# Kernel optimization log

Measured on AMD Instinct MI355X. Metric: run time of the kernel, lower is better.

## Reference

```python
import jax, jax.numpy as jnp
import numpy as np

B = 131072       # batch of sentences
L = 64           # padded paragraph length
N_TOPICS = 81    # topics 0..80 (range(81) in the original)


def setup_inputs() -> dict:
    key = jax.random.key(0)
    k1, k2, k3 = jax.random.split(key, 3)
    P = jax.random.uniform(k1, (B, N_TOPICS), dtype=jnp.float32)
    # -1 is the padding value; valid topic ids are in [0, 81)
    hard_label = jax.random.randint(k2, (B, L), -1, N_TOPICS, dtype=jnp.int64)
    sent_idx = jax.random.randint(k3, (B,), 0, 32, dtype=jnp.int64)
    return {"P": P, "hard_label": hard_label, "sent_idx": sent_idx}


def reference(P, hard_label, sent_idx):
    # mask1 = hard_label >= 0; mask1[0:sent_idx] = False
    pos = jnp.arange(L)
    mask = (hard_label >= 0) & (pos[None, :] >= sent_idx[:, None])  # [B, L]
    # set membership over topics 0..80: scatter masked labels into slot 81 (dump)
    valid = jnp.where(mask, hard_label, N_TOPICS)  # [B, L], invalid -> 81
    member = jnp.zeros((B, N_TOPICS + 1), dtype=bool)
    member = member.at[jnp.arange(B)[:, None], valid].set(True)[:, :N_TOPICS]  # [B, 81]
    # max_prob starts at 0 and only updated when P[i] > max_prob -> max(0, masked max)
    max_prob = jnp.max(jnp.where(member, P, 0.0), axis=1, initial=0.0)  # [B]
    return -max_prob
```

## Files before the change

kernel.cpp:

```cpp
#include <hip/hip_runtime.h>
#include <hip/hip_bf16.h>

#define L_LEN 64
#define N_TOPICS 81
#define ROW_STRIDE 84
#define ROWS_PER_WAVE 8
#define WAVES_PER_BLOCK 4
#define ROWS_PER_BLOCK 32

__global__ __launch_bounds__(256) void rangeshrink_max_kernel(
    const float* __restrict__ P,
    const int* __restrict__ hard_label,
    const int* __restrict__ sent_idx,
    float* __restrict__ out,
    int nrows)
{
    __shared__ float member[ROWS_PER_BLOCK * ROW_STRIDE];

    const int wave = threadIdx.x >> 6;
    const int lane = threadIdx.x & 63;
    const int g    = lane >> 3;
    const int lig  = lane & 7;

    const int localRow = wave * ROWS_PER_WAVE + g;
    const int row = blockIdx.x * ROWS_PER_BLOCK + localRow;
    if (row >= nrows) return;

    const float* __restrict__ Prow = P + (size_t)row * N_TOPICS;
    float pv[11];
    #pragma unroll
    for (int t = 0; t < 11; ++t) {
        const int idx = lig + 8 * t;
        pv[t] = (idx <= 80) ? Prow[idx] : 0.0f;
    }

    const int4* __restrict__ hl4 = (const int4*)hard_label;
    const int4 la = hl4[(size_t)row * 16 + lig * 2];
    const int4 lb = hl4[(size_t)row * 16 + lig * 2 + 1];
    const int si = sent_idx[row];

    float* const mwave = member + (wave * ROWS_PER_WAVE) * ROW_STRIDE;
    #pragma unroll
    for (int t = 0; t < 11; ++t) {
        const int d = lane + 64 * t;
        if (d < ROWS_PER_WAVE * ROW_STRIDE) mwave[d] = 0.0f;
    }
    __builtin_amdgcn_wave_barrier();

    float* const srow = member + localRow * ROW_STRIDE;
    const int labs[8] = { la.x, la.y, la.z, la.w, lb.x, lb.y, lb.z, lb.w };
    #pragma unroll
    for (int k = 0; k < 8; ++k) {
        const int j = lig * 8 + k;
        if (j >= si && labs[k] >= 0) srow[labs[k]] = 1.0f;
    }
    __builtin_amdgcn_wave_barrier();

    const float* const mrow = member + localRow * ROW_STRIDE;
    float v = 0.0f;
    #pragma unroll
    for (int t = 0; t < 11; ++t) {
        const int idx = lig + 8 * t;
        if (idx <= 80) v = fmaxf(v, mrow[idx] * pv[t]);
    }

    #pragma unroll
    for (int off = 1; off < 8; off <<= 1) {
        v = fmaxf(v, __shfl_xor(v, off, 64));
    }

    if (lig == 0) out[row] = -v;
}

extern "C" void kernel_launch(void* const* d_in, const int* in_sizes, int n_in,
                              void* d_out, int out_size, void* d_ws, size_t ws_size,
                              hipStream_t stream) {
    const float* P          = (const float*)d_in[0];
    const int*   hard_label = (const int*)d_in[1];
    const int*   sent_idx   = (const int*)d_in[2];
    float*       out        = (float*)d_out;

    const int nrows = out_size;
    const int grid = (nrows + ROWS_PER_BLOCK - 1) / ROWS_PER_BLOCK;

    rangeshrink_max_kernel<<<grid, 256, 0, stream>>>(P, hard_label, sent_idx, out, nrows);
}
```

Baseline: 17.13 us.

## Replace shared-memory membership table with register bitmasks and float4 P loads

Builds the topic membership set as three 32-bit register bitmasks, OR-reduced across the 8 lanes of each row with shuffles, which removes the shared-memory zeroing, scatter and readback. P rows are now read as aligned float4 vectors from a 16-byte-aligned base, and the mask is shifted by the row's misalignment so each lane can pick its 4-bit nibble per vector. This cuts LDS traffic and the number of load instructions, but adds shift and bit arithmetic plus extra shuffles, and relies on careful bounds logic for the final row.

```diff
diff --git a/kernel.cpp b/kernel.cpp
--- a/kernel.cpp
+++ b/kernel.cpp
@@ -3,9 +3,7 @@
 
 #define L_LEN 64
 #define N_TOPICS 81
-#define ROW_STRIDE 84
 #define ROWS_PER_WAVE 8
-#define WAVES_PER_BLOCK 4
 #define ROWS_PER_BLOCK 32
 
 __global__ __launch_bounds__(256) void rangeshrink_max_kernel(
@@ -15,58 +13,77 @@
     float* __restrict__ out,
     int nrows)
 {
-    __shared__ float member[ROWS_PER_BLOCK * ROW_STRIDE];
-
     const int wave = threadIdx.x >> 6;
     const int lane = threadIdx.x & 63;
     const int g    = lane >> 3;
     const int lig  = lane & 7;
 
-    const int localRow = wave * ROWS_PER_WAVE + g;
-    const int row = blockIdx.x * ROWS_PER_BLOCK + localRow;
+    const int row = blockIdx.x * ROWS_PER_BLOCK + wave * ROWS_PER_WAVE + g;
     if (row >= nrows) return;
 
-    const float* __restrict__ Prow = P + (size_t)row * N_TOPICS;
-    float pv[11];
-    #pragma unroll
-    for (int t = 0; t < 11; ++t) {
-        const int idx = lig + 8 * t;
-        pv[t] = (idx <= 80) ? Prow[idx] : 0.0f;
-    }
+    const size_t base_dw = (size_t)row * N_TOPICS;
+    const int    off     = row & 3;
+    const size_t a0      = base_dw - off;
+    const float4* __restrict__ W4 = (const float4*)(P + a0);
+
+    const int f2 = lig + 16;
+    const bool ok2 = (f2 <= 20) && ((row < nrows - 1) || (4 * f2 + 3 <= 80 + off));
+
+    float4 p0 = W4[lig];
+    float4 p1 = W4[lig + 8];
+    float4 p2 = ok2 ? W4[f2] : make_float4(0.f, 0.f, 0.f, 0.f);
 
     const int4* __restrict__ hl4 = (const int4*)hard_label;
     const int4 la = hl4[(size_t)row * 16 + lig * 2];
     const int4 lb = hl4[(size_t)row * 16 + lig * 2 + 1];
-    const int si = sent_idx[row];
+    const int  si = sent_idx[row];
 
-    float* const mwave = member + (wave * ROWS_PER_WAVE) * ROW_STRIDE;
-    #pragma unroll
-    for (int t = 0; t < 11; ++t) {
-        const int d = lane + 64 * t;
-        if (d < ROWS_PER_WAVE * ROW_STRIDE) mwave[d] = 0.0f;
-    }
-    __builtin_amdgcn_wave_barrier();
-
-    float* const srow = member + localRow * ROW_STRIDE;
+    unsigned m0 = 0u, m1 = 0u, m2 = 0u;
     const int labs[8] = { la.x, la.y, la.z, la.w, lb.x, lb.y, lb.z, lb.w };
     #pragma unroll
     for (int k = 0; k < 8; ++k) {
-        const int j = lig * 8 + k;
-        if (j >= si && labs[k] >= 0) srow[labs[k]] = 1.0f;
-    }
-    __builtin_amdgcn_wave_barrier();
-
-    const float* const mrow = member + localRow * ROW_STRIDE;
-    float v = 0.0f;
-    #pragma unroll
-    for (int t = 0; t < 11; ++t) {
-        const int idx = lig + 8 * t;
-        if (idx <= 80) v = fmaxf(v, mrow[idx] * pv[t]);
+        const int j   = lig * 8 + k;
+        const int lab = labs[k];
+        const bool valid = (j >= si) && (lab >= 0);
+        const unsigned b = 1u << (lab & 31);
+        const int w = lab >> 5;
+        m0 |= (valid && w == 0) ? b : 0u;
+        m1 |= (valid && w == 1) ? b : 0u;
+        m2 |= (valid && w == 2) ? b : 0u;
     }
 
     #pragma unroll
-    for (int off = 1; off < 8; off <<= 1) {
-        v = fmaxf(v, __shfl_xor(v, off, 64));
+    for (int o = 1; o < 8; o <<= 1) {
+        m0 |= __shfl_xor(m0, o, 64);
+        m1 |= __shfl_xor(m1, o, 64);
+        m2 |= __shfl_xor(m2, o, 64);
+    }
+
+    const unsigned long long lo = (unsigned long long)m0 | ((unsigned long long)m1 << 32);
+    const unsigned long long hi = (unsigned long long)m1 | ((unsigned long long)m2 << 32);
+    const unsigned long long slo = lo << off;
+    const unsigned s0 = (unsigned)slo;
+    const unsigned s1 = (unsigned)(slo >> 32);
+    const unsigned s2 = (unsigned)((hi << off) >> 32);
+
+    const unsigned n0 = (s0 >> (4 * lig)) & 0xFu;
+    const unsigned n1 = (s1 >> (4 * lig)) & 0xFu;
+    const unsigned n2 = (s2 >> (4 * lig)) & 0xFu;
+
+    float v = 0.0f;
+    const float e0[4] = { p0.x, p0.y, p0.z, p0.w };
+    const float e1[4] = { p1.x, p1.y, p1.z, p1.w };
+    const float e2[4] = { p2.x, p2.y, p2.z, p2.w };
+    #pragma unroll
+    for (int e = 0; e < 4; ++e) {
+        v = fmaxf(v, ((n0 >> e) & 1u) ? e0[e] : 0.0f);
+        v = fmaxf(v, ((n1 >> e) & 1u) ? e1[e] : 0.0f);
+        v = fmaxf(v, ((n2 >> e) & 1u) ? e2[e] : 0.0f);
+    }
+
+    #pragma unroll
+    for (int o = 1; o < 8; o <<= 1) {
+        v = fmaxf(v, __shfl_xor(v, o, 64));
     }
 
     if (lig == 0) out[row] = -v;
```

After: 18.01 us. +5.1%, slower.

## Stage P rows in LDS and gather by label instead of building membership mask

Applied to the files above, without the earlier changes.

Each row's P values are now loaded with aligned float4 reads and written into LDS, and each lane gathers P at its masked labels directly, taking the max. This removes the membership-mask zeroing pass, the scattered flag writes and one wave barrier, and replaces scalar P loads with vector loads. In exchange it adds boundary logic for unaligned row starts, including an over-read guard on the last row, and a trash slot that absorbs out-of-range stores.

```diff
diff --git a/kernel.cpp b/kernel.cpp
--- a/kernel.cpp
+++ b/kernel.cpp
@@ -1,12 +1,12 @@
 #include <hip/hip_runtime.h>
 #include <hip/hip_bf16.h>
 
-#define L_LEN 64
 #define N_TOPICS 81
-#define ROW_STRIDE 84
 #define ROWS_PER_WAVE 8
-#define WAVES_PER_BLOCK 4
 #define ROWS_PER_BLOCK 32
+#define ROW_STRIDE 88
+#define ZERO_SLOT 84
+#define TRASH_SLOT 86
 
 __global__ __launch_bounds__(256) void rangeshrink_max_kernel(
     const float* __restrict__ P,
@@ -15,7 +15,7 @@
     float* __restrict__ out,
     int nrows)
 {
-    __shared__ float member[ROWS_PER_BLOCK * ROW_STRIDE];
+    __shared__ float lds[ROWS_PER_BLOCK * ROW_STRIDE];
 
     const int wave = threadIdx.x >> 6;
     const int lane = threadIdx.x & 63;
@@ -26,47 +26,52 @@
     const int row = blockIdx.x * ROWS_PER_BLOCK + localRow;
     if (row >= nrows) return;
 
-    const float* __restrict__ Prow = P + (size_t)row * N_TOPICS;
-    float pv[11];
-    #pragma unroll
-    for (int t = 0; t < 11; ++t) {
-        const int idx = lig + 8 * t;
-        pv[t] = (idx <= 80) ? Prow[idx] : 0.0f;
-    }
+    const size_t base_dw = (size_t)row * N_TOPICS;
+    const int    off     = (int)(base_dw & 3);
+    const float4* __restrict__ W4 = (const float4*)(P + (base_dw - off));
+
+    float4 p0 = W4[lig];
+    float4 p1 = W4[lig + 8];
+    float4 p2 = make_float4(0.f, 0.f, 0.f, 0.f);
+    const bool ok2 = (lig <= 4) && ((row < nrows - 1) || (off == 3));
+    if (ok2) p2 = W4[lig + 16];
 
     const int4* __restrict__ hl4 = (const int4*)hard_label;
     const int4 la = hl4[(size_t)row * 16 + lig * 2];
     const int4 lb = hl4[(size_t)row * 16 + lig * 2 + 1];
-    const int si = sent_idx[row];
+    const int  si = sent_idx[row];
 
-    float* const mwave = member + (wave * ROWS_PER_WAVE) * ROW_STRIDE;
+    float* const srow = lds + localRow * ROW_STRIDE;
+    if (lig == 0) srow[ZERO_SLOT] = 0.0f;
+
+    const int d0 = lig * 4 - off;
+    const float pe0[4] = { p0.x, p0.y, p0.z, p0.w };
+    const float pe1[4] = { p1.x, p1.y, p1.z, p1.w };
+    const float pe2[4] = { p2.x, p2.y, p2.z, p2.w };
     #pragma unroll
-    for (int t = 0; t < 11; ++t) {
-        const int d = lane + 64 * t;
-        if (d < ROWS_PER_WAVE * ROW_STRIDE) mwave[d] = 0.0f;
+    for (int e = 0; e < 4; ++e) {
+        const int t0 = d0 + e;
+        srow[((unsigned)t0 <= 80u) ? t0 : TRASH_SLOT] = pe0[e];
+        const int t1 = d0 + 32 + e;
+        srow[t1] = pe1[e];
+        const int t2 = d0 + 64 + e;
+        srow[((unsigned)t2 <= 80u) ? t2 : TRASH_SLOT] = pe2[e];
     }
     __builtin_amdgcn_wave_barrier();
 
-    float* const srow = member + localRow * ROW_STRIDE;
+    const int base = lig * 8 - si;
     const int labs[8] = { la.x, la.y, la.z, la.w, lb.x, lb.y, lb.z, lb.w };
+    float v = 0.0f;
     #pragma unroll
     for (int k = 0; k < 8; ++k) {
-        const int j = lig * 8 + k;
-        if (j >= si && labs[k] >= 0) srow[labs[k]] = 1.0f;
-    }
-    __builtin_amdgcn_wave_barrier();
-
-    const float* const mrow = member + localRow * ROW_STRIDE;
-    float v = 0.0f;
-    #pragma unroll
-    for (int t = 0; t < 11; ++t) {
-        const int idx = lig + 8 * t;
-        if (idx <= 80) v = fmaxf(v, mrow[idx] * pv[t]);
+        const int m   = (base + k) | labs[k];
+        const int idx = (m < 0) ? ZERO_SLOT : labs[k];
+        v = fmaxf(v, srow[idx]);
     }
 
     #pragma unroll
-    for (int off = 1; off < 8; off <<= 1) {
-        v = fmaxf(v, __shfl_xor(v, off, 64));
+    for (int o = 1; o < 8; o <<= 1) {
+        v = fmaxf(v, __shfl_xor(v, o, 64));
     }
 
     if (lig == 0) out[row] = -v;
```

Result: no change. 17.26 us (+0.7%).
